# Kernel optimization log

Measured on AMD Instinct MI355X. Metric: run time of the kernel, lower is better.

Reference implementation:

```python
import jax, jax.numpy as jnp
import numpy as np

B, N, DIN, DOUT = 8, 2048, 256, 256

def setup_inputs() -> dict:
    key = jax.random.key(0)
    k1, k2, k3 = jax.random.split(key, 3)
    H = jax.random.normal(k1, (B, N, DIN), dtype=jnp.float32)
    G = jax.random.uniform(k2, (B, N, N), dtype=jnp.float32)  # positive -> nonzero row/col sums
    # xavier_uniform-style scale for the weight
    limit = float(np.sqrt(6.0 / (DIN + DOUT)))
    W = jax.random.uniform(k3, (DIN, DOUT), dtype=jnp.float32, minval=-limit, maxval=limit)
    return {"H": H, "G": G, "W": W}

def reference(H, G, W):
    # N_e = H @ W : [b,n,dout]
    N_e = H @ W
    # symmetric part
    G_F = (G + jnp.swapaxes(G, 1, 2)) * 0.5
    # loop over k of outer products == two normalized Gram matrices:
    # G_Sin[i,j] = sum_k G[k,i]*G[k,j] / rowsum_k  == G^T diag(1/rowsum) G
    # G_So[i,j]  = sum_k G[i,k]*G[j,k] / colsum_k  == G diag(1/colsum) G^T
    rs = G.sum(axis=-1)  # [b,n] row sums
    cs = G.sum(axis=-2)  # [b,n] col sums
    G_Sin = jnp.einsum('bki,bkj->bij', G / rs[:, :, None], G)
    G_So = jnp.einsum('bik,bjk->bij', G / cs[:, None, :], G)
    H_out = jnp.concatenate([
        jax.nn.relu(G_F @ N_e),
        jax.nn.relu(G_Sin @ N_e),
        jax.nn.relu(G_So @ N_e),
    ], axis=-1)  # [b,n,3*dout]
    return H_out
```

## Files before the change

### kernel.cpp

```cpp
#include <hip/hip_runtime.h>
#include <hip/hip_bf16.h>


constexpr int NN = 2048;
constexpr long GSTR = (long)NN * NN;

using frag8   = __attribute__((ext_vector_type(8))) short;
using floatx4 = __attribute__((ext_vector_type(4))) float;
using ush8    = __attribute__((ext_vector_type(8))) unsigned short;

__device__ inline unsigned short f2bf(float x) {
    unsigned u = __float_as_uint(x);
    u += 0x7FFF + ((u >> 16) & 1);
    return (unsigned short)(u >> 16);
}
__device__ inline float bf2f(unsigned short h) {
    return __uint_as_float((unsigned)h << 16);
}
__device__ inline ushort2 pk2(float a, float b) {
    union { __hip_bfloat162 h; ushort2 u; } cv;
    cv.h = __float22bfloat162_rn(float2{a, b});
    return cv.u;
}
__device__ inline void gload_lds16(const void* g, void* l) {
    __builtin_amdgcn_global_load_lds(
        (const __attribute__((address_space(1))) void*)g,
        (__attribute__((address_space(3))) void*)l, 16, 0, 0);
}

enum { EPI_NE = 0, EPI_M1 = 1, EPI_P2 = 2, EPI_O3 = 3 };

template <int EPI, int TM, int WJ, int NJ>
__global__ __launch_bounds__(256) void mgemm(
    const unsigned short* __restrict__ Aptr,
    const unsigned short* __restrict__ B0,
    const unsigned short* __restrict__ B1,
    const float* __restrict__ rsraw,
    unsigned short* __restrict__ CsT,
    float* __restrict__ outp,
    const float* __restrict__ scale,
    int K, long strideA, long sB)
{
    constexpr int MF = TM / 32;
    constexpr int NF = WJ / 32;
    __shared__ __align__(16) unsigned short As[2][TM * 64];
    __shared__ __align__(16) unsigned short Bs[2][WJ * 64];

    const int t  = threadIdx.x;
    const int bx = blockIdx.x;
    const int xcd = bx & 7;
    const int kk  = bx >> 3;
    constexpr int PER = NJ * 8;
    const int itile = xcd + 8 * (kk / PER);
    const int rem   = kk & (PER - 1);
    const int bb    = rem / NJ;
    const int jt    = rem & (NJ - 1);
    const int i0b = itile * TM;
    const int j0  = jt * WJ;

    const unsigned short* Btb =
        ((EPI == EPI_P2 && j0 >= 256) ? B1 + (long)(j0 - 256) * K
                                      : B0 + (long)j0 * K) + (long)bb * sB;
    const unsigned short* Ab = Aptr + (long)bb * strideA;

    const int w = t >> 6, l = t & 63;
    const int wm = w >> 1, wn = w & 1;
    const int quad = l >> 4, c15 = l & 15;

    const int lr  = l >> 3, ls = l & 7;

    floatx4 acc[MF][NF] = {};

    const int NT = K >> 6;

    auto stage = [&](int buf, int k0) {
        const unsigned short* Au = Ab + (((long)itile * (K >> 7) + (k0 >> 7)) << 14);
        const int kin = k0 & 127;
        #pragma unroll
        for (int q = 0; q < TM / 32; ++q) {
            const int rt = q * 32 + w * 8;
            gload_lds16(Au + (rt + lr) * 128 + kin + ((ls ^ lr) << 3),
                        &As[buf][rt * 64]);
        }
        #pragma unroll
        for (int q = 0; q < WJ / 32; ++q) {
            const int rt = q * 32 + w * 8;
            gload_lds16(Btb + (long)(rt + lr) * K + k0 + ((ls ^ lr) << 3),
                        &Bs[buf][rt * 64]);
        }
    };

    stage(0, 0);
    asm volatile("s_waitcnt vmcnt(0)" ::: "memory");
    __builtin_amdgcn_s_barrier();
    __builtin_amdgcn_sched_barrier(0);

    int cur = 0;
    for (int tt = 0; tt < NT; ++tt) {
        if (tt + 1 < NT) stage(cur ^ 1, (tt + 1) << 6);
        __builtin_amdgcn_sched_barrier(0);

        #pragma unroll
        for (int ks = 0; ks < 2; ++ks) {
            frag8 af[MF], bfv[NF];
            const int swr = c15 & 7;
            #pragma unroll
            for (int mt = 0; mt < MF; ++mt)
                af[mt] = *(const frag8*)&As[cur][(wm * (TM / 2) + mt * 16 + c15) * 64
                                               + (((ks * 4 + quad) ^ swr) << 3)];
            #pragma unroll
            for (int nt = 0; nt < NF; ++nt)
                bfv[nt] = *(const frag8*)&Bs[cur][(wn * (WJ / 2) + nt * 16 + c15) * 64
                                                + (((ks * 4 + quad) ^ swr) << 3)];
            #pragma unroll
            for (int mt = 0; mt < MF; ++mt)
                #pragma unroll
                for (int nt = 0; nt < NF; ++nt)
                    acc[mt][nt] = __builtin_amdgcn_mfma_f32_16x16x32_bf16(
                        af[mt], bfv[nt], acc[mt][nt], 0, 0, 0);
        }

        if (tt + 1 < NT) {
            asm volatile("s_waitcnt vmcnt(0)" ::: "memory");
            __builtin_amdgcn_s_barrier();
            __builtin_amdgcn_sched_barrier(0);
        }
        cur ^= 1;
    }

    const long rowb = (long)bb * NN;
    #pragma unroll
    for (int mt = 0; mt < MF; ++mt) {
        const int il = wm * (TM / 2) + mt * 16 + quad * 4;
        const int ib = i0b + il;
        float4 s4 = make_float4(1.f, 1.f, 1.f, 1.f);
        if constexpr (EPI == EPI_M1) s4 = *(const float4*)(scale + rowb + ib);
        if constexpr (EPI == EPI_P2) {
            if (j0 < 256) s4 = *(const float4*)(scale + rowb + ib);
        }
        #pragma unroll
        for (int nt = 0; nt < NF; ++nt) {
            floatx4 v = acc[mt][nt];
            const int gj = j0 + wn * (WJ / 2) + nt * 16 + c15;
            if constexpr (EPI == EPI_NE) {
                union { ushort4 v; ushort2 u2[2]; } p;
                p.u2[0] = pk2(v[0], v[1]); p.u2[1] = pk2(v[2], v[3]);
                *(ushort4*)(CsT + ((long)bb * 256 + gj) * 2048 + ib) = p.v;
            } else if constexpr (EPI == EPI_M1) {
                union { ushort4 v; ushort2 u2[2]; } p;
                p.u2[0] = pk2(v[0] * s4.x, v[1] * s4.y);
                p.u2[1] = pk2(v[2] * s4.z, v[3] * s4.w);
                *(ushort4*)(CsT + ((long)bb * 256 + gj) * 2048 + ib) = p.v;
            } else if constexpr (EPI == EPI_P2) {
                if (j0 < 256) {
                    union { ushort4 v; ushort2 u2[2]; } p;
                    p.u2[0] = pk2(v[0] * s4.x, v[1] * s4.y);
                    p.u2[1] = pk2(v[2] * s4.z, v[3] * s4.w);
                    *(ushort4*)(CsT + ((long)bb * 256 + gj) * 2048 + ib) = p.v;
                    const float4 rr = *(const float4*)(rsraw + rowb + ib);
                    const ushort4 m1p = *(const ushort4*)(B1 + ((long)bb * 256 + gj) * 2048 + ib);
                    const float m1v[4] = {bf2f(m1p.x) * rr.x, bf2f(m1p.y) * rr.y,
                                          bf2f(m1p.z) * rr.z, bf2f(m1p.w) * rr.w};
                    #pragma unroll
                    for (int r = 0; r < 4; ++r)
                        outp[(rowb + ib + r) * 768 + gj] = fmaxf(0.5f * (v[r] + m1v[r]), 0.f);
                } else {
                    #pragma unroll
                    for (int r = 0; r < 4; ++r)
                        outp[(rowb + ib + r) * 768 + gj] = fmaxf(v[r], 0.f);
                }
            } else {
                #pragma unroll
                for (int r = 0; r < 4; ++r)
                    outp[(rowb + ib + r) * 768 + 512 + gj] = fmaxf(v[r], 0.f);
            }
        }
    }
}

__global__ __launch_bounds__(256) void cvt_stream(
    const float* __restrict__ G,
    unsigned short* __restrict__ Gbf,
    float* __restrict__ pcs,
    float* __restrict__ inv_rs, float* __restrict__ rs_raw)
{
    __shared__ float sm[4][16];
    const int b  = blockIdx.y;
    const int s  = blockIdx.x;
    const int i0 = s * 16;
    const int t  = threadIdx.x;
    const int c8 = t * 8;
    const int w  = t >> 6, l = t & 63;

    const float* gp = G + (long)b * GSTR + (long)i0 * NN + c8;
    unsigned short* gb = Gbf + (long)b * GSTR;
    const int tc = c8 >> 7, cin = c8 & 127;

    float csum[8] = {};
    float rp[16];

    #pragma unroll
    for (int r = 0; r < 16; ++r) {
        const float4 x0 = *(const float4*)(gp + (long)r * NN);
        const float4 x1 = *(const float4*)(gp + (long)r * NN + 4);
        union { ush8 v; ushort2 u2[4]; } pk;
        pk.u2[0] = pk2(x0.x, x0.y); pk.u2[1] = pk2(x0.z, x0.w);
        pk.u2[2] = pk2(x1.x, x1.y); pk.u2[3] = pk2(x1.z, x1.w);
        const int gi = i0 + r;
        *(ush8*)(gb + (((long)(gi >> 7) * 16 + tc) << 14) + ((gi & 127) << 7) + cin) = pk.v;
        rp[r] = x0.x + x0.y + x0.z + x0.w + x1.x + x1.y + x1.z + x1.w;
        csum[0] += x0.x; csum[1] += x0.y; csum[2] += x0.z; csum[3] += x0.w;
        csum[4] += x1.x; csum[5] += x1.y; csum[6] += x1.z; csum[7] += x1.w;
    }

    float* pp = pcs + ((long)b * 128 + s) * NN + c8;
    *(float4*)pp       = make_float4(csum[0], csum[1], csum[2], csum[3]);
    *(float4*)(pp + 4) = make_float4(csum[4], csum[5], csum[6], csum[7]);

    #pragma unroll
    for (int r = 0; r < 16; ++r) {
        rp[r] += __shfl_xor(rp[r], 1);
        rp[r] += __shfl_xor(rp[r], 2);
        rp[r] += __shfl_xor(rp[r], 4);
        rp[r] += __shfl_xor(rp[r], 8);
        rp[r] += __shfl_xor(rp[r], 16);
        rp[r] += __shfl_xor(rp[r], 32);
    }
    if (l == 0) {
        #pragma unroll
        for (int r = 0; r < 16; ++r) sm[w][r] = rp[r];
    }
    __syncthreads();
    if (t < 16) {
        const float s_ = sm[0][t] + sm[1][t] + sm[2][t] + sm[3][t];
        rs_raw[(long)b * NN + i0 + t] = s_;
        inv_rs[(long)b * NN + i0 + t] = 1.0f / s_;
    }
}

__global__ __launch_bounds__(256) void cvt_t(
    const unsigned short* __restrict__ Gbf, unsigned short* __restrict__ GbfT)
{
    const int b  = blockIdx.z;
    const int tr = blockIdx.y, tc = blockIdx.x;
    const long src = (long)b * GSTR + (((long)tr * 16 + tc) << 14);
    const long dst = (long)b * GSTR + (((long)tc * 16 + tr) << 14);
    const int t = threadIdx.x;
    const int w = t >> 6, l = t & 63;
    const int wm = w >> 1, wn = w & 1;
    const int rg = l >> 3, c = l & 7;
    const int il = wm * 64 + rg * 8;
    const int jl = wn * 64 + c * 8;

    union RowU { ush8 v; unsigned u4[4]; };
    RowU rows[8], cols[8];
    #pragma unroll
    for (int r = 0; r < 8; ++r)
        rows[r].v = *(const ush8*)(Gbf + src + (long)(il + r) * 128 + jl);
    __builtin_amdgcn_sched_barrier(0);

    #pragma unroll
    for (int p = 0; p < 4; ++p) {
        #pragma unroll
        for (int k = 0; k < 4; ++k) {
            const unsigned a = rows[2 * p].u4[k], bq = rows[2 * p + 1].u4[k];
            cols[2 * k].u4[p]     = (a & 0xffffu) | (bq << 16);
            cols[2 * k + 1].u4[p] = (a >> 16) | (bq & 0xffff0000u);
        }
    }
    #pragma unroll
    for (int j = 0; j < 8; ++j)
        *(ush8*)(GbfT + dst + (long)(jl + j) * 128 + il) = cols[j].v;
}

__global__ __launch_bounds__(256) void cvt_h(
    const float* __restrict__ H, unsigned short* __restrict__ Hbf)
{
    const int b = blockIdx.y, it = blockIdx.x;
    const int t = threadIdx.x;
    const int rsub = t >> 5, c = (t & 31) * 8;
    const float* hp = H + ((long)b * 2048 + (long)it * 128) * 256;
    unsigned short* ob = Hbf + (long)b * (2048L * 256) + (((long)it * 2 + (c >> 7)) << 14);
    const int cin = c & 127;
    #pragma unroll
    for (int rr = 0; rr < 16; ++rr) {
        const int r = rr * 8 + rsub;
        const float4 x0 = *(const float4*)(hp + (long)r * 256 + c);
        const float4 x1 = *(const float4*)(hp + (long)r * 256 + c + 4);
        union { ush8 v; ushort2 u2[4]; } pk;
        pk.u2[0] = pk2(x0.x, x0.y); pk.u2[1] = pk2(x0.z, x0.w);
        pk.u2[2] = pk2(x1.x, x1.y); pk.u2[3] = pk2(x1.z, x1.w);
        *(ush8*)(ob + r * 128 + cin) = pk.v;
    }
}

__global__ __launch_bounds__(256) void finalize(
    const float* __restrict__ pcs,
    float* __restrict__ inv_cs,
    const float* __restrict__ W, unsigned short* __restrict__ Wt)
{
    const int idx = blockIdx.x * 256 + threadIdx.x;
    if (blockIdx.y == 0) {
        const int b = idx >> 11, i = idx & 2047;
        float s = 0.f;
        for (int ic = 0; ic < 128; ++ic) s += pcs[((long)b * 128 + ic) * NN + i];
        inv_cs[idx] = 1.0f / s;
    } else {
        #pragma unroll
        for (int e = 0; e < 4; ++e) {
            const int flat = idx * 4 + e;
            const int j = flat >> 8, k = flat & 255;
            Wt[flat] = f2bf(W[(long)k * 256 + j]);
        }
    }
}

extern "C" void kernel_launch(void* const* d_in, const int* in_sizes, int n_in,
                              void* d_out, int out_size, void* d_ws, size_t ws_size,
                              hipStream_t stream)
{
    constexpr int B = 8;
    const float* H = (const float*)d_in[0];
    const float* G = (const float*)d_in[1];
    const float* W = (const float*)d_in[2];
    float* out = (float*)d_out;

    unsigned short* ws16 = (unsigned short*)d_ws;
    unsigned short* Gbf  = ws16;
    unsigned short* GbfT = Gbf  + (long)B * GSTR;
    unsigned short* Wt   = GbfT + (long)B * GSTR;
    unsigned short* NeT  = Wt   + 65536;
    unsigned short* M1sT = NeT  + 4194304;
    unsigned short* M2sT = M1sT + 4194304;
    unsigned short* Hbf  = M2sT + 4194304;
    float* inv_rs = (float*)(Hbf + 4194304);
    float* rs_raw = inv_rs + 16384;
    float* inv_cs = rs_raw + 16384;
    float* pcs    = inv_cs + 16384;

    cvt_stream<<<dim3(128, 8), 256, 0, stream>>>(G, Gbf, pcs, inv_rs, rs_raw);
    cvt_t<<<dim3(16, 16, 8), 256, 0, stream>>>(Gbf, GbfT);
    cvt_h<<<dim3(16, 8), 256, 0, stream>>>(H, Hbf);
    finalize<<<dim3(64, 2), 256, 0, stream>>>(pcs, inv_cs, W, Wt);

    const long sNT = 256L * NN;
    mgemm<EPI_NE, 128, 64, 4><<<512, 256, 0, stream>>>(
        Hbf, Wt, nullptr, nullptr, NeT, nullptr, nullptr,
        256, 2048L * 256, 0);
    mgemm<EPI_M1, 128, 64, 4><<<512, 256, 0, stream>>>(
        Gbf, NeT, nullptr, nullptr, M1sT, nullptr, inv_rs,
        2048, GSTR, sNT);
    mgemm<EPI_P2, 128, 128, 4><<<512, 256, 0, stream>>>(
        GbfT, NeT, M1sT, rs_raw, M2sT, out, inv_cs,
        2048, GSTR, sNT);
    mgemm<EPI_O3, 128, 64, 4><<<512, 256, 0, stream>>>(
        Gbf, M2sT, nullptr, nullptr, nullptr, out, nullptr,
        2048, GSTR, sNT);
}
```

Before: 373.7 us.

## Restructure Gram GEMM chain into transposed-output phases with LDS-staged epilogues

Replaces the four chained GEMMs with two symmetric phases. The first phase computes both the G^T(Ne) and G(Ne) scaled intermediates in one launch. The second phase computes the Sin and So outputs by multiplying the intermediates against G or G^T, with N-dim tiles of 256 rows and K=2048. The G_F branch is rebuilt by a separate elementwise kernel from the two intermediates rescaled by the raw row and column sums, which removes a full dependent N×N×D GEMM. Epilogues go through LDS transposes to get coalesced stores. In exchange, bf16 rounding now sits on a different path for G_F, and LDS use per block is larger.

```diff
diff --git a/kernel.cpp b/kernel.cpp
--- a/kernel.cpp
+++ b/kernel.cpp
@@ -4,6 +4,7 @@
 
 constexpr int NN = 2048;
 constexpr long GSTR = (long)NN * NN;
+constexpr long SDN = 256L * 2048;
 
 using frag8   = __attribute__((ext_vector_type(8))) short;
 using floatx4 = __attribute__((ext_vector_type(4))) float;
@@ -28,62 +29,235 @@
         (__attribute__((address_space(3))) void*)l, 16, 0, 0);
 }
 
-enum { EPI_NE = 0, EPI_M1 = 1, EPI_P2 = 2, EPI_O3 = 3 };
-
-template <int EPI, int TM, int WJ, int NJ>
-__global__ __launch_bounds__(256) void mgemm(
-    const unsigned short* __restrict__ Aptr,
-    const unsigned short* __restrict__ B0,
-    const unsigned short* __restrict__ B1,
-    const float* __restrict__ rsraw,
-    unsigned short* __restrict__ CsT,
+template <int PHASE>
+__global__ __launch_bounds__(256) void gemmF(
+    const unsigned short* __restrict__ Aa,
+    const unsigned short* __restrict__ Ab,
+    const unsigned short* __restrict__ Gb,
+    const unsigned short* __restrict__ GbT,
+    unsigned short* __restrict__ C0,
+    unsigned short* __restrict__ C1,
     float* __restrict__ outp,
-    const float* __restrict__ scale,
-    int K, long strideA, long sB)
-{
-    constexpr int MF = TM / 32;
-    constexpr int NF = WJ / 32;
+    const float* __restrict__ s0,
+    const float* __restrict__ s1)
+{
+    constexpr int TM = 256, NT = 32;
+    __shared__ __align__(16) unsigned short SH[2][(TM + 64) * 64];
+
+    const int bx = blockIdx.x;
+    const int bb = bx & 7;
+    const int rr_ = bx >> 3;
+    const int jt = rr_ & 31;
+    const int h  = rr_ >> 5;
+    const int j0 = jt * 64;
+
+    const unsigned short* Ap =
+        ((PHASE == 1 && h) ? Ab : Aa) + (long)bb * SDN;
+    const unsigned short* Bp =
+        (((PHASE == 0) == (h == 0)) ? Gb : GbT) + (long)bb * GSTR;
+
+    const int t = threadIdx.x;
+    const int w = t >> 6, l = t & 63;
+    const int wm = w >> 1, wn = w & 1;
+    const int quad = l >> 4, c15 = l & 15;
+    const int lr = l >> 3, ls = l & 7;
+
+    floatx4 acc[8][2] = {};
+
+    auto stage = [&](int buf, int k0) {
+        #pragma unroll
+        for (int q = 0; q < 8; ++q) {
+            const int rt = q * 32 + w * 8;
+            gload_lds16(Ap + (long)(rt + lr) * 2048 + k0 + ((ls ^ lr) << 3),
+                        &SH[buf][rt * 64]);
+        }
+        const unsigned short* Bt = Bp + (((long)(j0 >> 7) * 16 + (k0 >> 7)) << 14);
+        const int rb = j0 & 127, kin = k0 & 127;
+        #pragma unroll
+        for (int q = 0; q < 2; ++q) {
+            const int rt = q * 32 + w * 8;
+            gload_lds16(Bt + (rb + rt + lr) * 128 + kin + ((ls ^ lr) << 3),
+                        &SH[buf][TM * 64 + rt * 64]);
+        }
+    };
+
+    stage(0, 0);
+    asm volatile("s_waitcnt vmcnt(0)" ::: "memory");
+    __builtin_amdgcn_s_barrier();
+    __builtin_amdgcn_sched_barrier(0);
+
+    int cur = 0;
+    for (int tt = 0; tt < NT; ++tt) {
+        if (tt + 1 < NT) stage(cur ^ 1, (tt + 1) << 6);
+        __builtin_amdgcn_sched_barrier(0);
+        #pragma unroll
+        for (int ks = 0; ks < 2; ++ks) {
+            frag8 af[8], bfv[2];
+            const int swr = c15 & 7;
+            #pragma unroll
+            for (int mt = 0; mt < 8; ++mt)
+                af[mt] = *(const frag8*)&SH[cur][(wm * 128 + mt * 16 + c15) * 64
+                                                + (((ks * 4 + quad) ^ swr) << 3)];
+            #pragma unroll
+            for (int nt = 0; nt < 2; ++nt)
+                bfv[nt] = *(const frag8*)&SH[cur][TM * 64 + (wn * 32 + nt * 16 + c15) * 64
+                                                 + (((ks * 4 + quad) ^ swr) << 3)];
+            #pragma unroll
+            for (int mt = 0; mt < 8; ++mt)
+                #pragma unroll
+                for (int nt = 0; nt < 2; ++nt)
+                    acc[mt][nt] = __builtin_amdgcn_mfma_f32_16x16x32_bf16(
+                        af[mt], bfv[nt], acc[mt][nt], 0, 0, 0);
+        }
+        if (tt + 1 < NT) {
+            asm volatile("s_waitcnt vmcnt(0)" ::: "memory");
+            __builtin_amdgcn_s_barrier();
+            __builtin_amdgcn_sched_barrier(0);
+        }
+        cur ^= 1;
+    }
+
+    __syncthreads();
+
+    if constexpr (PHASE == 0) {
+        unsigned short* T16 = &SH[0][0];
+        #pragma unroll
+        for (int nt = 0; nt < 2; ++nt) {
+            const int jc = wn * 32 + nt * 16 + c15;
+            const float sc = (h ? s1 : s0)[(long)bb * 2048 + j0 + jc];
+            #pragma unroll
+            for (int mt = 0; mt < 8; ++mt) {
+                const floatx4 v = acc[mt][nt];
+                const int ib = wm * 128 + mt * 16 + quad * 4;
+                #pragma unroll
+                for (int e = 0; e < 4; ++e)
+                    T16[(ib + e) * 72 + jc] = f2bf(v[e] * sc);
+            }
+        }
+        __syncthreads();
+        unsigned short* Co = (h ? C1 : C0) + ((long)bb * 256 + t) * 2048 + j0;
+        const unsigned short* Tr = T16 + t * 72;
+        #pragma unroll
+        for (int c2 = 0; c2 < 8; ++c2)
+            *(ush8*)(Co + c2 * 8) = *(const ush8*)(Tr + c2 * 8);
+    } else {
+        float* TF = (float*)&SH[0][0];
+        #pragma unroll
+        for (int nt = 0; nt < 2; ++nt) {
+            const int jc = wn * 32 + nt * 16 + c15;
+            #pragma unroll
+            for (int mt = 0; mt < 8; ++mt) {
+                const floatx4 v = acc[mt][nt];
+                const int ib = wm * 128 + mt * 16 + quad * 4;
+                #pragma unroll
+                for (int e = 0; e < 4; ++e)
+                    TF[jc * 260 + ib + e] = fmaxf(v[e], 0.f);
+            }
+        }
+        __syncthreads();
+        const int jr = t >> 2, iq = t & 3;
+        float* Op = outp + ((long)bb * 2048 + j0 + jr) * 768 + (h ? 512 : 256) + iq * 64;
+        const float* Sp = TF + jr * 260 + iq * 64;
+        #pragma unroll
+        for (int c2 = 0; c2 < 16; ++c2)
+            *(float4*)(Op + c2 * 4) = *(const float4*)(Sp + c2 * 4);
+    }
+}
+
+__global__ __launch_bounds__(256) void out0k(
+    const unsigned short* __restrict__ M1sT, const unsigned short* __restrict__ M2sT,
+    const float* __restrict__ rs_raw, const float* __restrict__ cs_raw,
+    float* __restrict__ outp)
+{
+    const int bb = blockIdx.y, jt = blockIdx.x;
+    const int j0 = jt * 64;
+    const int t = threadIdx.x;
+    const int w = t >> 6, l = t & 63;
+    const int rg = l >> 3, c = l & 7;
+    const int ib = w * 64 + rg * 8;
+    const int jb = j0 + c * 8;
+    const long ab = (long)bb * SDN;
+
+    union RowU { ush8 v; unsigned u4[4]; unsigned short a[8]; };
+    RowU r1[8], r2[8], c1[8], c2[8];
+    #pragma unroll
+    for (int r = 0; r < 8; ++r) {
+        r1[r].v = *(const ush8*)(M1sT + ab + (long)(ib + r) * 2048 + jb);
+        r2[r].v = *(const ush8*)(M2sT + ab + (long)(ib + r) * 2048 + jb);
+    }
+    __builtin_amdgcn_sched_barrier(0);
+    #pragma unroll
+    for (int p = 0; p < 4; ++p)
+        #pragma unroll
+        for (int k = 0; k < 4; ++k) {
+            const unsigned a1 = r1[2*p].u4[k], b1 = r1[2*p+1].u4[k];
+            c1[2*k].u4[p]   = (a1 & 0xffffu) | (b1 << 16);
+            c1[2*k+1].u4[p] = (a1 >> 16) | (b1 & 0xffff0000u);
+            const unsigned a2 = r2[2*p].u4[k], b2 = r2[2*p+1].u4[k];
+            c2[2*k].u4[p]   = (a2 & 0xffffu) | (b2 << 16);
+            c2[2*k+1].u4[p] = (a2 >> 16) | (b2 & 0xffff0000u);
+        }
+    #pragma unroll
+    for (int jj = 0; jj < 8; ++jj) {
+        const int j = jb + jj;
+        const float rr = rs_raw[(long)bb * 2048 + j];
+        const float cc = cs_raw[(long)bb * 2048 + j];
+        float4 o0, o1;
+        o0.x = fmaxf(0.5f * (bf2f(c1[jj].a[0]) * rr + bf2f(c2[jj].a[0]) * cc), 0.f);
+        o0.y = fmaxf(0.5f * (bf2f(c1[jj].a[1]) * rr + bf2f(c2[jj].a[1]) * cc), 0.f);
+        o0.z = fmaxf(0.5f * (bf2f(c1[jj].a[2]) * rr + bf2f(c2[jj].a[2]) * cc), 0.f);
+        o0.w = fmaxf(0.5f * (bf2f(c1[jj].a[3]) * rr + bf2f(c2[jj].a[3]) * cc), 0.f);
+        o1.x = fmaxf(0.5f * (bf2f(c1[jj].a[4]) * rr + bf2f(c2[jj].a[4]) * cc), 0.f);
+        o1.y = fmaxf(0.5f * (bf2f(c1[jj].a[5]) * rr + bf2f(c2[jj].a[5]) * cc), 0.f);
+        o1.z = fmaxf(0.5f * (bf2f(c1[jj].a[6]) * rr + bf2f(c2[jj].a[6]) * cc), 0.f);
+        o1.w = fmaxf(0.5f * (bf2f(c1[jj].a[7]) * rr + bf2f(c2[jj].a[7]) * cc), 0.f);
+        float* op = outp + ((long)bb * 2048 + j) * 768 + ib;
+        *(float4*)op       = o0;
+        *(float4*)(op + 4) = o1;
+    }
+}
+
+__global__ __launch_bounds__(256) void gemmNE(
+    const unsigned short* __restrict__ Hbf,
+    const unsigned short* __restrict__ Wt,
+    unsigned short* __restrict__ NeT)
+{
+    constexpr int TM = 128, K = 256, NT = 4;
     __shared__ __align__(16) unsigned short As[2][TM * 64];
-    __shared__ __align__(16) unsigned short Bs[2][WJ * 64];
+    __shared__ __align__(16) unsigned short Bs[2][64 * 64];
 
     const int t  = threadIdx.x;
     const int bx = blockIdx.x;
     const int xcd = bx & 7;
     const int kk  = bx >> 3;
-    constexpr int PER = NJ * 8;
-    const int itile = xcd + 8 * (kk / PER);
-    const int rem   = kk & (PER - 1);
-    const int bb    = rem / NJ;
-    const int jt    = rem & (NJ - 1);
+    const int itile = xcd + 8 * (kk >> 5);
+    const int rem   = kk & 31;
+    const int bb    = rem >> 2;
+    const int jt    = rem & 3;
     const int i0b = itile * TM;
-    const int j0  = jt * WJ;
-
-    const unsigned short* Btb =
-        ((EPI == EPI_P2 && j0 >= 256) ? B1 + (long)(j0 - 256) * K
-                                      : B0 + (long)j0 * K) + (long)bb * sB;
-    const unsigned short* Ab = Aptr + (long)bb * strideA;
+    const int j0  = jt * 64;
+
+    const unsigned short* Btb = Wt + (long)j0 * K;
+    const unsigned short* Ab  = Hbf + (long)bb * SDN;
 
     const int w = t >> 6, l = t & 63;
     const int wm = w >> 1, wn = w & 1;
     const int quad = l >> 4, c15 = l & 15;
-
-    const int lr  = l >> 3, ls = l & 7;
-
-    floatx4 acc[MF][NF] = {};
-
-    const int NT = K >> 6;
+    const int lr = l >> 3, ls = l & 7;
+
+    floatx4 acc[4][2] = {};
 
     auto stage = [&](int buf, int k0) {
-        const unsigned short* Au = Ab + (((long)itile * (K >> 7) + (k0 >> 7)) << 14);
+        const unsigned short* Au = Ab + (((long)itile * 2 + (k0 >> 7)) << 14);
         const int kin = k0 & 127;
         #pragma unroll
-        for (int q = 0; q < TM / 32; ++q) {
+        for (int q = 0; q < 4; ++q) {
             const int rt = q * 32 + w * 8;
             gload_lds16(Au + (rt + lr) * 128 + kin + ((ls ^ lr) << 3),
                         &As[buf][rt * 64]);
         }
         #pragma unroll
-        for (int q = 0; q < WJ / 32; ++q) {
+        for (int q = 0; q < 2; ++q) {
             const int rt = q * 32 + w * 8;
             gload_lds16(Btb + (long)(rt + lr) * K + k0 + ((ls ^ lr) << 3),
                         &Bs[buf][rt * 64]);
@@ -99,27 +273,25 @@
     for (int tt = 0; tt < NT; ++tt) {
         if (tt + 1 < NT) stage(cur ^ 1, (tt + 1) << 6);
         __builtin_amdgcn_sched_barrier(0);
-
         #pragma unroll
         for (int ks = 0; ks < 2; ++ks) {
-            frag8 af[MF], bfv[NF];
+            frag8 af[4], bfv[2];
             const int swr = c15 & 7;
             #pragma unroll
-            for (int mt = 0; mt < MF; ++mt)
-                af[mt] = *(const frag8*)&As[cur][(wm * (TM / 2) + mt * 16 + c15) * 64
+            for (int mt = 0; mt < 4; ++mt)
+                af[mt] = *(const frag8*)&As[cur][(wm * 64 + mt * 16 + c15) * 64
                                                + (((ks * 4 + quad) ^ swr) << 3)];
             #pragma unroll
-            for (int nt = 0; nt < NF; ++nt)
-                bfv[nt] = *(const frag8*)&Bs[cur][(wn * (WJ / 2) + nt * 16 + c15) * 64
+            for (int nt = 0; nt < 2; ++nt)
+                bfv[nt] = *(const frag8*)&Bs[cur][(wn * 32 + nt * 16 + c15) * 64
                                                 + (((ks * 4 + quad) ^ swr) << 3)];
             #pragma unroll
-            for (int mt = 0; mt < MF; ++mt)
+            for (int mt = 0; mt < 4; ++mt)
                 #pragma unroll
-                for (int nt = 0; nt < NF; ++nt)
+                for (int nt = 0; nt < 2; ++nt)
                     acc[mt][nt] = __builtin_amdgcn_mfma_f32_16x16x32_bf16(
                         af[mt], bfv[nt], acc[mt][nt], 0, 0, 0);
         }
-
         if (tt + 1 < NT) {
             asm volatile("s_waitcnt vmcnt(0)" ::: "memory");
             __builtin_amdgcn_s_barrier();
@@ -128,52 +300,16 @@
         cur ^= 1;
     }
 
-    const long rowb = (long)bb * NN;
-    #pragma unroll
-    for (int mt = 0; mt < MF; ++mt) {
-        const int il = wm * (TM / 2) + mt * 16 + quad * 4;
-        const int ib = i0b + il;
-        float4 s4 = make_float4(1.f, 1.f, 1.f, 1.f);
-        if constexpr (EPI == EPI_M1) s4 = *(const float4*)(scale + rowb + ib);
-        if constexpr (EPI == EPI_P2) {
-            if (j0 < 256) s4 = *(const float4*)(scale + rowb + ib);
-        }
-        #pragma unroll
-        for (int nt = 0; nt < NF; ++nt) {
-            floatx4 v = acc[mt][nt];
-            const int gj = j0 + wn * (WJ / 2) + nt * 16 + c15;
-            if constexpr (EPI == EPI_NE) {
-                union { ushort4 v; ushort2 u2[2]; } p;
-                p.u2[0] = pk2(v[0], v[1]); p.u2[1] = pk2(v[2], v[3]);
-                *(ushort4*)(CsT + ((long)bb * 256 + gj) * 2048 + ib) = p.v;
-            } else if constexpr (EPI == EPI_M1) {
-                union { ushort4 v; ushort2 u2[2]; } p;
-                p.u2[0] = pk2(v[0] * s4.x, v[1] * s4.y);
-                p.u2[1] = pk2(v[2] * s4.z, v[3] * s4.w);
-                *(ushort4*)(CsT + ((long)bb * 256 + gj) * 2048 + ib) = p.v;
-            } else if constexpr (EPI == EPI_P2) {
-                if (j0 < 256) {
-                    union { ushort4 v; ushort2 u2[2]; } p;
-                    p.u2[0] = pk2(v[0] * s4.x, v[1] * s4.y);
-                    p.u2[1] = pk2(v[2] * s4.z, v[3] * s4.w);
-                    *(ushort4*)(CsT + ((long)bb * 256 + gj) * 2048 + ib) = p.v;
-                    const float4 rr = *(const float4*)(rsraw + rowb + ib);
-                    const ushort4 m1p = *(const ushort4*)(B1 + ((long)bb * 256 + gj) * 2048 + ib);
-                    const float m1v[4] = {bf2f(m1p.x) * rr.x, bf2f(m1p.y) * rr.y,
-                                          bf2f(m1p.z) * rr.z, bf2f(m1p.w) * rr.w};
-                    #pragma unroll
-                    for (int r = 0; r < 4; ++r)
-                        outp[(rowb + ib + r) * 768 + gj] = fmaxf(0.5f * (v[r] + m1v[r]), 0.f);
-                } else {
-                    #pragma unroll
-                    for (int r = 0; r < 4; ++r)
-                        outp[(rowb + ib + r) * 768 + gj] = fmaxf(v[r], 0.f);
-                }
-            } else {
-                #pragma unroll
-                for (int r = 0; r < 4; ++r)
-                    outp[(rowb + ib + r) * 768 + 512 + gj] = fmaxf(v[r], 0.f);
-            }
+    #pragma unroll
+    for (int mt = 0; mt < 4; ++mt) {
+        const int ib = i0b + wm * 64 + mt * 16 + quad * 4;
+        #pragma unroll
+        for (int nt = 0; nt < 2; ++nt) {
+            const floatx4 v = acc[mt][nt];
+            const int gj = j0 + wn * 32 + nt * 16 + c15;
+            union { ushort4 v; ushort2 u2[2]; } p;
+            p.u2[0] = pk2(v[0], v[1]); p.u2[1] = pk2(v[2], v[3]);
+            *(ushort4*)(NeT + ((long)bb * 256 + gj) * 2048 + ib) = p.v;
         }
     }
 }
@@ -260,14 +396,13 @@
     __builtin_amdgcn_sched_barrier(0);
 
     #pragma unroll
-    for (int p = 0; p < 4; ++p) {
+    for (int p = 0; p < 4; ++p)
         #pragma unroll
         for (int k = 0; k < 4; ++k) {
             const unsigned a = rows[2 * p].u4[k], bq = rows[2 * p + 1].u4[k];
             cols[2 * k].u4[p]     = (a & 0xffffu) | (bq << 16);
             cols[2 * k + 1].u4[p] = (a >> 16) | (bq & 0xffff0000u);
         }
-    }
     #pragma unroll
     for (int j = 0; j < 8; ++j)
         *(ush8*)(GbfT + dst + (long)(jl + j) * 128 + il) = cols[j].v;
@@ -280,7 +415,7 @@
     const int t = threadIdx.x;
     const int rsub = t >> 5, c = (t & 31) * 8;
     const float* hp = H + ((long)b * 2048 + (long)it * 128) * 256;
-    unsigned short* ob = Hbf + (long)b * (2048L * 256) + (((long)it * 2 + (c >> 7)) << 14);
+    unsigned short* ob = Hbf + (long)b * SDN + (((long)it * 2 + (c >> 7)) << 14);
     const int cin = c & 127;
     #pragma unroll
     for (int rr = 0; rr < 16; ++rr) {
@@ -296,7 +431,7 @@
 
 __global__ __launch_bounds__(256) void finalize(
     const float* __restrict__ pcs,
-    float* __restrict__ inv_cs,
+    float* __restrict__ inv_cs, float* __restrict__ cs_raw,
     const float* __restrict__ W, unsigned short* __restrict__ Wt)
 {
     const int idx = blockIdx.x * 256 + threadIdx.x;
@@ -305,6 +440,7 @@
         float s = 0.f;
         for (int ic = 0; ic < 128; ++ic) s += pcs[((long)b * 128 + ic) * NN + i];
         inv_cs[idx] = 1.0f / s;
+        cs_raw[idx] = s;
     } else {
         #pragma unroll
         for (int e = 0; e < 4; ++e) {
@@ -336,24 +472,18 @@
     float* inv_rs = (float*)(Hbf + 4194304);
     float* rs_raw = inv_rs + 16384;
     float* inv_cs = rs_raw + 16384;
-    float* pcs    = inv_cs + 16384;
+    float* cs_raw = inv_cs + 16384;
+    float* pcs    = cs_raw + 16384;
 
     cvt_stream<<<dim3(128, 8), 256, 0, stream>>>(G, Gbf, pcs, inv_rs, rs_raw);
     cvt_t<<<dim3(16, 16, 8), 256, 0, stream>>>(Gbf, GbfT);
     cvt_h<<<dim3(16, 8), 256, 0, stream>>>(H, Hbf);
-    finalize<<<dim3(64, 2), 256, 0, stream>>>(pcs, inv_cs, W, Wt);
-
-    const long sNT = 256L * NN;
-    mgemm<EPI_NE, 128, 64, 4><<<512, 256, 0, stream>>>(
-        Hbf, Wt, nullptr, nullptr, NeT, nullptr, nullptr,
-        256, 2048L * 256, 0);
-    mgemm<EPI_M1, 128, 64, 4><<<512, 256, 0, stream>>>(
-        Gbf, NeT, nullptr, nullptr, M1sT, nullptr, inv_rs,
-        2048, GSTR, sNT);
-    mgemm<EPI_P2, 128, 128, 4><<<512, 256, 0, stream>>>(
-        GbfT, NeT, M1sT, rs_raw, M2sT, out, inv_cs,
-        2048, GSTR, sNT);
-    mgemm<EPI_O3, 128, 64, 4><<<512, 256, 0, stream>>>(
-        Gbf, M2sT, nullptr, nullptr, nullptr, out, nullptr,
-        2048, GSTR, sNT);
-}
+    finalize<<<dim3(64, 2), 256, 0, stream>>>(pcs, inv_cs, cs_raw, W, Wt);
+
+    gemmNE<<<512, 256, 0, stream>>>(Hbf, Wt, NeT);
+    gemmF<0><<<512, 256, 0, stream>>>(NeT, nullptr, Gbf, GbfT,
+                                      M1sT, M2sT, nullptr, inv_rs, inv_cs);
+    gemmF<1><<<512, 256, 0, stream>>>(M1sT, M2sT, Gbf, GbfT,
+                                      nullptr, nullptr, out, nullptr, nullptr);
+    out0k<<<dim3(32, 8), 256, 0, stream>>>(M1sT, M2sT, rs_raw, cs_raw, out);
+}
```

New measurement: 358.4 us. 1.04x faster.
